# Kernel tuning notes

Measured on AMD Instinct MI355X. Metric: run time of the kernel, lower is better.

The kernel has to match this reference:

```python
import jax, jax.numpy as jnp
import numpy as np

N = 100000
E = 1600000
F_IN = 32
HID = 16


def _sage_conv(x, src, dst, W_l, b_l, W_r):
    # PyG SAGEConv (aggr='mean', normalize=False, root_weight=True):
    #   out = lin_l(mean_{j in N(i)} x_j) + lin_r(x_i)
    # lin_l has bias, lin_r has no bias.
    n = x.shape[0]
    msg_sum = jax.ops.segment_sum(x[src], dst, num_segments=n)          # [N, d]
    deg = jax.ops.segment_sum(jnp.ones_like(dst, dtype=x.dtype), dst, num_segments=n)
    agg = msg_sum / jnp.maximum(deg, 1.0)[:, None]                      # mean, 0 for isolated nodes
    return agg @ W_l.T + b_l + x @ W_r.T


def setup_inputs() -> dict:
    key = jax.random.key(0)
    ks = jax.random.split(key, 8)
    x = jax.random.normal(ks[0], (N, F_IN), dtype=jnp.float32)
    edge_index = jax.random.randint(ks[1], (1, 2, E), 0, N, dtype=jnp.int64)
    s1 = 1.0 / np.sqrt(F_IN)
    s2 = 1.0 / np.sqrt(HID)
    W1_l = jax.random.uniform(ks[2], (HID, F_IN), jnp.float32, -s1, s1)
    b1_l = jax.random.uniform(ks[3], (HID,), jnp.float32, -s1, s1)
    W1_r = jax.random.uniform(ks[4], (HID, F_IN), jnp.float32, -s1, s1)
    W2_l = jax.random.uniform(ks[5], (F_IN, HID), jnp.float32, -s2, s2)
    b2_l = jax.random.uniform(ks[6], (F_IN,), jnp.float32, -s2, s2)
    W2_r = jax.random.uniform(ks[7], (F_IN, HID), jnp.float32, -s2, s2)
    return {"x": x, "edge_index": edge_index, "W1_l": W1_l, "b1_l": b1_l,
            "W1_r": W1_r, "W2_l": W2_l, "b2_l": b2_l, "W2_r": W2_r}


def reference(x, edge_index, W1_l, b1_l, W1_r, W2_l, b2_l, W2_r):
    ei = jnp.squeeze(edge_index, axis=0)  # [2, E]
    src, dst = ei[0], ei[1]
    h = jax.nn.relu(_sage_conv(x, src, dst, W1_l, b1_l, W1_r))
    out = _sage_conv(h, src, dst, W2_l, b2_l, W2_r)
    return out
```

## Files before the change

kernel.cpp:

```cpp
#include <hip/hip_runtime.h>

#define F_IN 32
#define HID 16
#define BSHIFT 7
#define BNODES (1 << BSHIFT)
#define CAP 2560
#define CHUNK 8192
#define SRCM 0x1FFFFu
#define WS1 33
#define WS2 17

__device__ __forceinline__ void add4(float4& a, const float4& b) {
    a.x += b.x; a.y += b.y; a.z += b.z; a.w += b.w;
}
__device__ __forceinline__ unsigned pack2(float a, float b) {
    unsigned ua = __float_as_uint(a);
    unsigned ub = __float_as_uint(b);
    ua = (ua + 0x7FFFu + ((ua >> 16) & 1u)) >> 16;
    ub = (ub + 0x7FFFu + ((ub >> 16) & 1u)) >> 16;
    return ua | (ub << 16);
}
__device__ __forceinline__ float lo2f(unsigned u) { return __uint_as_float(u << 16); }
__device__ __forceinline__ float hi2f(unsigned u) { return __uint_as_float(u & 0xFFFF0000u); }
__device__ __forceinline__ float4 unp(uint2 v) {
    return make_float4(lo2f(v.x), hi2f(v.x), lo2f(v.y), hi2f(v.y));
}

__global__ void __launch_bounds__(256) k_pre(const float* __restrict__ x,
                                             const float* __restrict__ W1_l,
                                             unsigned* __restrict__ y1b,
                                             const int* __restrict__ ei,
                                             int* __restrict__ bucketCursor,
                                             unsigned* __restrict__ bucketBuf,
                                             int N, int E, int nodeBlocks) {
    __shared__ int cnt[1024];
    __shared__ int runBase[1024];
    __shared__ float Ws[HID * F_IN];
    int tid = threadIdx.x;

    if ((int)blockIdx.x < nodeBlocks) {
        for (int i = tid; i < HID * F_IN; i += 256) Ws[i] = W1_l[i];
        __syncthreads();
        int node = blockIdx.x * 256 + tid;
        if (node >= N) return;
        float xr[F_IN];
        const float4* xp = (const float4*)(x + (size_t)node * F_IN);
#pragma unroll
        for (int i = 0; i < F_IN / 4; i++) {
            float4 v = xp[i];
            xr[4 * i + 0] = v.x; xr[4 * i + 1] = v.y;
            xr[4 * i + 2] = v.z; xr[4 * i + 3] = v.w;
        }
        float a[HID];
#pragma unroll
        for (int o = 0; o < HID; o++) {
            float s = 0.f;
#pragma unroll
            for (int k = 0; k < F_IN; k++) s += xr[k] * Ws[o * F_IN + k];
            a[o] = s;
        }
        uint4* yp = (uint4*)(y1b + (size_t)node * 8);
        yp[0] = make_uint4(pack2(a[0], a[1]), pack2(a[2], a[3]),
                           pack2(a[4], a[5]), pack2(a[6], a[7]));
        yp[1] = make_uint4(pack2(a[8], a[9]), pack2(a[10], a[11]),
                           pack2(a[12], a[13]), pack2(a[14], a[15]));
        return;
    }

    int pb = blockIdx.x - nodeBlocks;
    int e0 = pb * CHUNK;
    int e1 = min(e0 + CHUNK, E);
    int n4 = (e1 - e0) >> 2;
    const int4* dst4 = (const int4*)(ei + E + e0);
    const int4* src4 = (const int4*)(ei + e0);

#pragma unroll
    for (int i = 0; i < 4; i++) cnt[tid + 256 * i] = 0;
    __syncthreads();
    for (int i = tid; i < n4; i += 256) {
        int4 d = dst4[i];
        atomicAdd(&cnt[d.x >> BSHIFT], 1);
        atomicAdd(&cnt[d.y >> BSHIFT], 1);
        atomicAdd(&cnt[d.z >> BSHIFT], 1);
        atomicAdd(&cnt[d.w >> BSHIFT], 1);
    }
    __syncthreads();
#pragma unroll
    for (int i = 0; i < 4; i++) {
        int b = tid + 256 * i;
        int c = cnt[b];
        runBase[b] = c ? atomicAdd(&bucketCursor[b], c) : 0;
        cnt[b] = 0;
    }
    __syncthreads();
    for (int i = tid; i < n4; i += 256) {
        int4 d = dst4[i];
        int4 s = src4[i];
        {
            int b = d.x >> BSHIFT;
            int pos = runBase[b] + atomicAdd(&cnt[b], 1);
            if (pos < CAP)
                bucketBuf[(size_t)b * CAP + pos] = ((unsigned)(d.x & (BNODES - 1)) << 17) | (unsigned)s.x;
        }
        {
            int b = d.y >> BSHIFT;
            int pos = runBase[b] + atomicAdd(&cnt[b], 1);
            if (pos < CAP)
                bucketBuf[(size_t)b * CAP + pos] = ((unsigned)(d.y & (BNODES - 1)) << 17) | (unsigned)s.y;
        }
        {
            int b = d.z >> BSHIFT;
            int pos = runBase[b] + atomicAdd(&cnt[b], 1);
            if (pos < CAP)
                bucketBuf[(size_t)b * CAP + pos] = ((unsigned)(d.z & (BNODES - 1)) << 17) | (unsigned)s.z;
        }
        {
            int b = d.w >> BSHIFT;
            int pos = runBase[b] + atomicAdd(&cnt[b], 1);
            if (pos < CAP)
                bucketBuf[(size_t)b * CAP + pos] = ((unsigned)(d.w & (BNODES - 1)) << 17) | (unsigned)s.w;
        }
    }
}

__global__ void __launch_bounds__(256) k_agg1f(const unsigned* __restrict__ y1b,
                                               const float* __restrict__ x,
                                               const unsigned* __restrict__ bucketBuf,
                                               const int* __restrict__ bucketCursor,
                                               const float* __restrict__ W1_r,
                                               const float* __restrict__ b1,
                                               unsigned* __restrict__ hb, int N) {
    __shared__ unsigned sA[CAP];
    __shared__ unsigned sB[CAP];
    __shared__ int hist[BNODES];
    __shared__ int scn[BNODES];
    __shared__ int cur[BNODES];
    __shared__ float Ws[HID * WS1];
    __shared__ float bs[HID];
    int tid = threadIdx.x, b = blockIdx.x;

    for (int i = tid; i < HID * F_IN; i += 256) Ws[(i >> 5) * WS1 + (i & 31)] = W1_r[i];
    if (tid < HID) bs[tid] = b1[tid];
    if (tid < BNODES) hist[tid] = 0;
    int nRec = min(bucketCursor[b], CAP);
    const unsigned* buf = bucketBuf + (size_t)b * CAP;
    for (int i = tid; i < nRec; i += 256) sA[i] = buf[i];
    __syncthreads();
    for (int i = tid; i < nRec; i += 256) atomicAdd(&hist[sA[i] >> 17], 1);
    __syncthreads();
    if (tid < BNODES) scn[tid] = hist[tid];
    __syncthreads();
    for (int off = 1; off < BNODES; off <<= 1) {
        int v = (tid < BNODES && tid >= off) ? scn[tid - off] : 0;
        __syncthreads();
        if (tid < BNODES && tid >= off) scn[tid] += v;
        __syncthreads();
    }
    if (tid < BNODES) cur[tid] = scn[tid] - hist[tid];
    __syncthreads();
    for (int i = tid; i < nRec; i += 256) {
        unsigned r = sA[i];
        int pos = atomicAdd(&cur[r >> 17], 1);
        sB[pos] = r & SRCM;
    }
    __syncthreads();

    const uint2* yv = (const uint2*)y1b;
#pragma unroll
    for (int pass = 0; pass < 2; pass++) {
        int slot = pass * 256 + tid;
        int nl = slot >> 2, c = slot & 3;
        int node = b * BNODES + nl;
        if (node >= N) continue;
        int start = scn[nl] - hist[nl];
        int dg = hist[nl];
        int jend = start + dg;
        float4 a0 = make_float4(0, 0, 0, 0), a1 = a0;
        int j = start;
        for (; j + 4 <= jend; j += 4) {
            unsigned s0 = sB[j], s1 = sB[j + 1], s2 = sB[j + 2], s3 = sB[j + 3];
            uint2 v0 = yv[(size_t)s0 * 4 + c];
            uint2 v1 = yv[(size_t)s1 * 4 + c];
            uint2 v2 = yv[(size_t)s2 * 4 + c];
            uint2 v3 = yv[(size_t)s3 * 4 + c];
            add4(a0, unp(v0)); add4(a1, unp(v1));
            add4(a0, unp(v2)); add4(a1, unp(v3));
        }
        for (; j < jend; j++) {
            uint2 v = yv[(size_t)sB[j] * 4 + c];
            add4(a0, unp(v));
        }
        add4(a0, a1);
        float inv = 1.0f / (float)(dg > 0 ? dg : 1);
        float m[4] = {a0.x * inv, a0.y * inv, a0.z * inv, a0.w * inv};

        float xr[F_IN];
        const float4* xp = (const float4*)(x + (size_t)node * F_IN);
#pragma unroll
        for (int q = 0; q < F_IN / 4; q++) {
            float4 v = xp[q];
            xr[4 * q + 0] = v.x; xr[4 * q + 1] = v.y;
            xr[4 * q + 2] = v.z; xr[4 * q + 3] = v.w;
        }
        float a[4];
#pragma unroll
        for (int jj = 0; jj < 4; jj++) {
            int o = c * 4 + jj;
            float s = m[jj] + bs[o];
#pragma unroll
            for (int k = 0; k < F_IN; k++) s += xr[k] * Ws[o * WS1 + k];
            a[jj] = fmaxf(s, 0.0f);
        }
        ((uint2*)hb)[(size_t)node * 4 + c] = make_uint2(pack2(a[0], a[1]), pack2(a[2], a[3]));
    }
}

__global__ void __launch_bounds__(256) k_l2f(const unsigned* __restrict__ hb,
                                             const unsigned* __restrict__ bucketBuf,
                                             const int* __restrict__ bucketCursor,
                                             const float* __restrict__ W2_l,
                                             const float* __restrict__ b2,
                                             const float* __restrict__ W2_r,
                                             float* __restrict__ out, int N) {
    __shared__ unsigned sA[CAP];
    __shared__ unsigned sB[CAP];
    __shared__ int hist[BNODES];
    __shared__ int scn[BNODES];
    __shared__ int cur[BNODES];
    __shared__ float Wl[F_IN * WS2];
    __shared__ float Wr[F_IN * WS2];
    __shared__ float bs[F_IN];
    int tid = threadIdx.x, b = blockIdx.x;

    for (int i = tid; i < F_IN * HID; i += 256) {
        int r = i >> 4, q = i & 15;
        Wl[r * WS2 + q] = W2_l[i];
        Wr[r * WS2 + q] = W2_r[i];
    }
    if (tid < F_IN) bs[tid] = b2[tid];
    if (tid < BNODES) hist[tid] = 0;
    int nRec = min(bucketCursor[b], CAP);
    const unsigned* buf = bucketBuf + (size_t)b * CAP;
    for (int i = tid; i < nRec; i += 256) sA[i] = buf[i];
    __syncthreads();
    for (int i = tid; i < nRec; i += 256) atomicAdd(&hist[sA[i] >> 17], 1);
    __syncthreads();
    if (tid < BNODES) scn[tid] = hist[tid];
    __syncthreads();
    for (int off = 1; off < BNODES; off <<= 1) {
        int v = (tid < BNODES && tid >= off) ? scn[tid - off] : 0;
        __syncthreads();
        if (tid < BNODES && tid >= off) scn[tid] += v;
        __syncthreads();
    }
    if (tid < BNODES) cur[tid] = scn[tid] - hist[tid];
    __syncthreads();
    for (int i = tid; i < nRec; i += 256) {
        unsigned r = sA[i];
        int pos = atomicAdd(&cur[r >> 17], 1);
        sB[pos] = r & SRCM;
    }
    __syncthreads();

    float* mm = (float*)sA;
    const uint2* hv = (const uint2*)hb;
#pragma unroll
    for (int pass = 0; pass < 2; pass++) {
        int slot = pass * 256 + tid;
        int nl = slot >> 2, c = slot & 3;
        int node = b * BNODES + nl;
        if (node >= N) continue;
        int start = scn[nl] - hist[nl];
        int dg = hist[nl];
        int jend = start + dg;
        float4 a0 = make_float4(0, 0, 0, 0), a1 = a0;
        int j = start;
        for (; j + 4 <= jend; j += 4) {
            unsigned s0 = sB[j], s1 = sB[j + 1], s2 = sB[j + 2], s3 = sB[j + 3];
            uint2 v0 = hv[(size_t)s0 * 4 + c];
            uint2 v1 = hv[(size_t)s1 * 4 + c];
            uint2 v2 = hv[(size_t)s2 * 4 + c];
            uint2 v3 = hv[(size_t)s3 * 4 + c];
            add4(a0, unp(v0)); add4(a1, unp(v1));
            add4(a0, unp(v2)); add4(a1, unp(v3));
        }
        for (; j < jend; j++) {
            uint2 v = hv[(size_t)sB[j] * 4 + c];
            add4(a0, unp(v));
        }
        add4(a0, a1);
        float inv = 1.0f / (float)(dg > 0 ? dg : 1);
        mm[nl * (HID + 1) + c * 4 + 0] = a0.x * inv;
        mm[nl * (HID + 1) + c * 4 + 1] = a0.y * inv;
        mm[nl * (HID + 1) + c * 4 + 2] = a0.z * inv;
        mm[nl * (HID + 1) + c * 4 + 3] = a0.w * inv;
    }
    __syncthreads();

#pragma unroll
    for (int pass = 0; pass < 2; pass++) {
        int slot = pass * 256 + tid;
        int nl = slot >> 2, c = slot & 3;
        int node = b * BNODES + nl;
        if (node >= N) continue;

        float m[HID];
#pragma unroll
        for (int k = 0; k < HID; k++) m[k] = mm[nl * (HID + 1) + k];

        float hr[HID];
        const uint4* hp = (const uint4*)(hb + (size_t)node * 8);
        uint4 u0 = hp[0], u1 = hp[1];
        hr[0] = lo2f(u0.x); hr[1] = hi2f(u0.x); hr[2] = lo2f(u0.y); hr[3] = hi2f(u0.y);
        hr[4] = lo2f(u0.z); hr[5] = hi2f(u0.z); hr[6] = lo2f(u0.w); hr[7] = hi2f(u0.w);
        hr[8] = lo2f(u1.x); hr[9] = hi2f(u1.x); hr[10] = lo2f(u1.y); hr[11] = hi2f(u1.y);
        hr[12] = lo2f(u1.z); hr[13] = hi2f(u1.z); hr[14] = lo2f(u1.w); hr[15] = hi2f(u1.w);

        float a[8];
#pragma unroll
        for (int jj = 0; jj < 8; jj++) {
            int o = c * 8 + jj;
            float s = bs[o];
#pragma unroll
            for (int k = 0; k < HID; k++)
                s += m[k] * Wl[o * WS2 + k] + hr[k] * Wr[o * WS2 + k];
            a[jj] = s;
        }
        float4* op = (float4*)(out + (size_t)node * F_IN + c * 8);
        op[0] = make_float4(a[0], a[1], a[2], a[3]);
        op[1] = make_float4(a[4], a[5], a[6], a[7]);
    }
}

extern "C" void kernel_launch(void* const* d_in, const int* in_sizes, int n_in,
                              void* d_out, int out_size, void* d_ws, size_t ws_size,
                              hipStream_t stream) {
    const float* x    = (const float*)d_in[0];
    const int*   ei   = (const int*)d_in[1];
    const float* W1_l = (const float*)d_in[2];
    const float* b1   = (const float*)d_in[3];
    const float* W1_r = (const float*)d_in[4];
    const float* W2_l = (const float*)d_in[5];
    const float* b2   = (const float*)d_in[6];
    const float* W2_r = (const float*)d_in[7];
    float* out = (float*)d_out;

    const int N = in_sizes[0] / F_IN;
    const int E = in_sizes[1] / 2;
    const int nbuckets = (N + BNODES - 1) >> BSHIFT;

    int* bucketCursor = (int*)d_ws;
    unsigned* bucketBuf = (unsigned*)(bucketCursor + 1024);
    unsigned* y1b = bucketBuf + (size_t)nbuckets * CAP;
    unsigned* hb  = y1b + (size_t)N * 8;

    hipMemsetAsync(bucketCursor, 0, 1024 * sizeof(int), stream);

    const int nodeBlocks = (N + 255) / 256;
    const int partBlocks = (E + CHUNK - 1) / CHUNK;

    k_pre<<<nodeBlocks + partBlocks, 256, 0, stream>>>(x, W1_l, y1b, ei,
                                                       bucketCursor, bucketBuf,
                                                       N, E, nodeBlocks);
    k_agg1f<<<nbuckets, 256, 0, stream>>>(y1b, x, bucketBuf, bucketCursor,
                                          W1_r, b1, hb, N);
    k_l2f<<<nbuckets, 256, 0, stream>>>(hb, bucketBuf, bucketCursor,
                                        W2_l, b2, W2_r, out, N);
}
```

Baseline: 157.8 us.

## Reuse layer-1 bucket sort in layer 2 via written-back sorted sources and offsets

k_agg1f now writes its per-bucket counting-sorted source list back into bucketBuf, plus per-node start/end offsets into a new meta array. k_l2f loads the pre-sorted list with vector loads and skips the histogram, scan and scatter entirely. Bucket loads also become uint4 vector copies. The cost is extra global writes in layer 1 and a dependence on in-place overwrite of bucketBuf and extra workspace space.

```diff
diff --git a/kernel.cpp b/kernel.cpp
--- a/kernel.cpp
+++ b/kernel.cpp
@@ -125,13 +125,14 @@
 
 __global__ void __launch_bounds__(256) k_agg1f(const unsigned* __restrict__ y1b,
                                                const float* __restrict__ x,
-                                               const unsigned* __restrict__ bucketBuf,
+                                               unsigned* __restrict__ bucketBuf,
                                                const int* __restrict__ bucketCursor,
                                                const float* __restrict__ W1_r,
                                                const float* __restrict__ b1,
-                                               unsigned* __restrict__ hb, int N) {
-    __shared__ unsigned sA[CAP];
-    __shared__ unsigned sB[CAP];
+                                               unsigned* __restrict__ hb,
+                                               int* __restrict__ meta, int N) {
+    __shared__ __align__(16) unsigned sA[CAP];
+    __shared__ __align__(16) unsigned sB[CAP];
     __shared__ int hist[BNODES];
     __shared__ int scn[BNODES];
     __shared__ int cur[BNODES];
@@ -143,8 +144,10 @@
     if (tid < HID) bs[tid] = b1[tid];
     if (tid < BNODES) hist[tid] = 0;
     int nRec = min(bucketCursor[b], CAP);
-    const unsigned* buf = bucketBuf + (size_t)b * CAP;
-    for (int i = tid; i < nRec; i += 256) sA[i] = buf[i];
+    unsigned* buf = bucketBuf + (size_t)b * CAP;
+    int n4s = (nRec + 3) >> 2;
+    for (int i = tid; i < n4s; i += 256)
+        ((uint4*)sA)[i] = ((const uint4*)buf)[i];
     __syncthreads();
     for (int i = tid; i < nRec; i += 256) atomicAdd(&hist[sA[i] >> 17], 1);
     __syncthreads();
@@ -164,6 +167,13 @@
         sB[pos] = r & SRCM;
     }
     __syncthreads();
+
+    for (int i = tid; i < n4s; i += 256)
+        ((uint4*)buf)[i] = ((const uint4*)sB)[i];
+    if (tid < BNODES) {
+        meta[(size_t)b * 256 + tid] = scn[tid] - hist[tid];
+        meta[(size_t)b * 256 + BNODES + tid] = scn[tid];
+    }
 
     const uint2* yv = (const uint2*)y1b;
 #pragma unroll
@@ -218,15 +228,15 @@
 __global__ void __launch_bounds__(256) k_l2f(const unsigned* __restrict__ hb,
                                              const unsigned* __restrict__ bucketBuf,
                                              const int* __restrict__ bucketCursor,
+                                             const int* __restrict__ meta,
                                              const float* __restrict__ W2_l,
                                              const float* __restrict__ b2,
                                              const float* __restrict__ W2_r,
                                              float* __restrict__ out, int N) {
-    __shared__ unsigned sA[CAP];
-    __shared__ unsigned sB[CAP];
-    __shared__ int hist[BNODES];
-    __shared__ int scn[BNODES];
-    __shared__ int cur[BNODES];
+    __shared__ __align__(16) unsigned sB[CAP];
+    __shared__ int s0[BNODES];
+    __shared__ int s1[BNODES];
+    __shared__ float mm[BNODES * (HID + 1)];
     __shared__ float Wl[F_IN * WS2];
     __shared__ float Wr[F_IN * WS2];
     __shared__ float bs[F_IN];
@@ -238,31 +248,16 @@
         Wr[r * WS2 + q] = W2_r[i];
     }
     if (tid < F_IN) bs[tid] = b2[tid];
-    if (tid < BNODES) hist[tid] = 0;
+    if (tid < BNODES) {
+        s0[tid] = meta[(size_t)b * 256 + tid];
+        s1[tid] = meta[(size_t)b * 256 + BNODES + tid];
+    }
     int nRec = min(bucketCursor[b], CAP);
-    const unsigned* buf = bucketBuf + (size_t)b * CAP;
-    for (int i = tid; i < nRec; i += 256) sA[i] = buf[i];
-    __syncthreads();
-    for (int i = tid; i < nRec; i += 256) atomicAdd(&hist[sA[i] >> 17], 1);
-    __syncthreads();
-    if (tid < BNODES) scn[tid] = hist[tid];
-    __syncthreads();
-    for (int off = 1; off < BNODES; off <<= 1) {
-        int v = (tid < BNODES && tid >= off) ? scn[tid - off] : 0;
-        __syncthreads();
-        if (tid < BNODES && tid >= off) scn[tid] += v;
-        __syncthreads();
-    }
-    if (tid < BNODES) cur[tid] = scn[tid] - hist[tid];
-    __syncthreads();
-    for (int i = tid; i < nRec; i += 256) {
-        unsigned r = sA[i];
-        int pos = atomicAdd(&cur[r >> 17], 1);
-        sB[pos] = r & SRCM;
-    }
-    __syncthreads();
-
-    float* mm = (float*)sA;
+    const uint4* bv = (const uint4*)(bucketBuf + (size_t)b * CAP);
+    int n4s = (nRec + 3) >> 2;
+    for (int i = tid; i < n4s; i += 256) ((uint4*)sB)[i] = bv[i];
+    __syncthreads();
+
     const uint2* hv = (const uint2*)hb;
 #pragma unroll
     for (int pass = 0; pass < 2; pass++) {
@@ -270,17 +265,17 @@
         int nl = slot >> 2, c = slot & 3;
         int node = b * BNODES + nl;
         if (node >= N) continue;
-        int start = scn[nl] - hist[nl];
-        int dg = hist[nl];
-        int jend = start + dg;
+        int start = s0[nl];
+        int jend = s1[nl];
+        int dg = jend - start;
         float4 a0 = make_float4(0, 0, 0, 0), a1 = a0;
         int j = start;
         for (; j + 4 <= jend; j += 4) {
-            unsigned s0 = sB[j], s1 = sB[j + 1], s2 = sB[j + 2], s3 = sB[j + 3];
-            uint2 v0 = hv[(size_t)s0 * 4 + c];
-            uint2 v1 = hv[(size_t)s1 * 4 + c];
-            uint2 v2 = hv[(size_t)s2 * 4 + c];
-            uint2 v3 = hv[(size_t)s3 * 4 + c];
+            unsigned v0i = sB[j], v1i = sB[j + 1], v2i = sB[j + 2], v3i = sB[j + 3];
+            uint2 v0 = hv[(size_t)v0i * 4 + c];
+            uint2 v1 = hv[(size_t)v1i * 4 + c];
+            uint2 v2 = hv[(size_t)v2i * 4 + c];
+            uint2 v3 = hv[(size_t)v3i * 4 + c];
             add4(a0, unp(v0)); add4(a1, unp(v1));
             add4(a0, unp(v2)); add4(a1, unp(v3));
         }
@@ -353,6 +348,7 @@
     unsigned* bucketBuf = (unsigned*)(bucketCursor + 1024);
     unsigned* y1b = bucketBuf + (size_t)nbuckets * CAP;
     unsigned* hb  = y1b + (size_t)N * 8;
+    int* meta = (int*)(hb + (size_t)N * 8);
 
     hipMemsetAsync(bucketCursor, 0, 1024 * sizeof(int), stream);
 
@@ -363,7 +359,7 @@
                                                        bucketCursor, bucketBuf,
                                                        N, E, nodeBlocks);
     k_agg1f<<<nbuckets, 256, 0, stream>>>(y1b, x, bucketBuf, bucketCursor,
-                                          W1_r, b1, hb, N);
-    k_l2f<<<nbuckets, 256, 0, stream>>>(hb, bucketBuf, bucketCursor,
+                                          W1_r, b1, hb, meta, N);
+    k_l2f<<<nbuckets, 256, 0, stream>>>(hb, bucketBuf, bucketCursor, meta,
                                         W2_l, b2, W2_r, out, N);
 }
```

Measured after the change: 152.0 us. 1.04x faster.
